# Kernel optimization log

Hardware: AMD Instinct MI355X
Metric: run time of the kernel (lower is better)

## Reference

```python
import jax, jax.numpy as jnp
import numpy as np

D_MODEL = 1024
NUM_HEADS = 16
DEPTH = D_MODEL // NUM_HEADS
B, S = 4, 2048


def setup_inputs() -> dict:
    key = jax.random.key(0)
    ks = jax.random.split(key, 11)
    sc = 1.0 / np.sqrt(D_MODEL)
    return {
        "query": jax.random.normal(ks[0], (B, S, D_MODEL), jnp.float32),
        "key_": jax.random.normal(ks[1], (B, S, D_MODEL), jnp.float32),
        "value": jax.random.normal(ks[2], (B, S, D_MODEL), jnp.float32),
        # torch Linear: y = x @ W.T + b, W shape [out, in]
        "Wq": jax.random.normal(ks[3], (D_MODEL, D_MODEL), jnp.float32) * sc,
        "bq": jax.random.normal(ks[4], (D_MODEL,), jnp.float32) * sc,
        "Wk": jax.random.normal(ks[5], (D_MODEL, D_MODEL), jnp.float32) * sc,
        "bk": jax.random.normal(ks[6], (D_MODEL,), jnp.float32) * sc,
        "Wv": jax.random.normal(ks[7], (D_MODEL, D_MODEL), jnp.float32) * sc,
        "bv": jax.random.normal(ks[8], (D_MODEL,), jnp.float32) * sc,
        "Wo": jax.random.normal(ks[9], (D_MODEL, D_MODEL), jnp.float32) * sc,
        "bo": jax.random.normal(ks[10], (D_MODEL,), jnp.float32) * sc,
    }


def _split_heads(x):
    # [B,S,D] -> [B,H,S,depth]
    b, s, _ = x.shape
    return x.reshape(b, s, NUM_HEADS, DEPTH).transpose(0, 2, 1, 3)


def reference(query, key_, value, Wq, bq, Wk, bk, Wv, bv, Wo, bo):
    Q = _split_heads(query @ Wq.T + bq)
    K = _split_heads(key_ @ Wk.T + bk)
    V = _split_heads(value @ Wv.T + bv)
    scale = 1.0 / jnp.sqrt(jnp.float32(DEPTH))
    scores = jnp.einsum("bhqd,bhkd->bhqk", Q, K) * scale  # [B,H,S,S]
    attention_weights = jax.nn.softmax(scores, axis=-1)
    out = jnp.einsum("bhqk,bhkd->bhqd", attention_weights, V)
    out = out.transpose(0, 2, 1, 3).reshape(query.shape[0], -1, D_MODEL)
    out = out @ Wo.T + bo
    return out, attention_weights
```

## Files before the change

### kernel.cpp

```cpp
#include <hip/hip_runtime.h>

#define NHEAD 16
#define SEQ 2048
#define DMODEL 1024
#define BB 4
#define MROWS (BB*SEQ)
#define NBH (BB*NHEAD)
#define NT (SEQ/32)

typedef float f32x4 __attribute__((ext_vector_type(4)));
typedef _Float16 f16x8 __attribute__((ext_vector_type(8)));
typedef _Float16 f16x4 __attribute__((ext_vector_type(4)));

static __device__ __forceinline__ f32x4 mfma16(f16x8 a, f16x8 b, f32x4 c) {
  return __builtin_amdgcn_mfma_f32_16x16x32_f16(a, b, c, 0, 0, 0);
}

static __device__ __forceinline__ void split2(float x, unsigned short& hi, unsigned short& lo) {
  _Float16 h = (_Float16)x;
  hi = __builtin_bit_cast(unsigned short, h);
  lo = __builtin_bit_cast(unsigned short, (_Float16)(x - (float)h));
}

static __device__ __forceinline__ void gload_lds16(const unsigned short* g, unsigned short* l) {
  __builtin_amdgcn_global_load_lds(
      (const __attribute__((address_space(1))) unsigned int*)g,
      (__attribute__((address_space(3))) unsigned int*)l, 16, 0, 0);
}

__global__ __launch_bounds__(256)
void round_f16(const float* __restrict__ src, unsigned short* __restrict__ dst, int n4)
{
  int i = blockIdx.x*256 + threadIdx.x;
  const int stride = gridDim.x*256;
  for (; i < n4; i += stride) {
    const float4 x = ((const float4*)src)[i];
    ushort4 h;
    h.x = __builtin_bit_cast(unsigned short, (_Float16)x.x);
    h.y = __builtin_bit_cast(unsigned short, (_Float16)x.y);
    h.z = __builtin_bit_cast(unsigned short, (_Float16)x.z);
    h.w = __builtin_bit_cast(unsigned short, (_Float16)x.w);
    ((ushort4*)dst)[i] = h;
  }
}

__global__ __launch_bounds__(256)
void split_f32(const float* __restrict__ src, unsigned short* __restrict__ hi,
               unsigned short* __restrict__ lo, int n4)
{
  int i = blockIdx.x*256 + threadIdx.x;
  const int stride = gridDim.x*256;
  for (; i < n4; i += stride) {
    const float4 x = ((const float4*)src)[i];
    ushort4 h, l;
    split2(x.x, h.x, l.x); split2(x.y, h.y, l.y);
    split2(x.z, h.z, l.z); split2(x.w, h.w, l.w);
    ((ushort4*)hi)[i] = h;
    ((ushort4*)lo)[i] = l;
  }
}

template<int MODE>
__global__ __launch_bounds__(256, 2)
void proj_gemm(const unsigned short* __restrict__ Xf,
               const unsigned short* __restrict__ Wh, const unsigned short* __restrict__ Wl,
               const float* __restrict__ bias, float oscale,
               unsigned short* __restrict__ o16, float* __restrict__ o_f32)
{
  __shared__ unsigned short As[128][32];
  __shared__ unsigned short Bs[128][64];
  const int tid  = threadIdx.x;
  const int wid  = tid >> 6, lane = tid & 63;
  const int g    = lane >> 4, r16 = lane & 15;
  const int id   = blockIdx.y*64 + blockIdx.x;
  const int xcd  = id & 7, slot = id >> 3;
  const int m0   = (xcd*8 + (slot & 7)) * 128;
  const int n0   = (slot >> 3) * 128;
  const int wr   = wid >> 1, wc = wid & 1;

  f32x4 acc[4][4] = {};

  for (int kt = 0; kt < 32; ++kt) {
    const int k0 = kt*32;
    __syncthreads();
#pragma unroll
    for (int r = 0; r < 2; ++r) {
      const int gi = r*256 + tid;
      const int row = gi >> 2, c = gi & 3;
      const int lg = c ^ ((row >> 1) & 3);
      gload_lds16(Xf + (size_t)(m0+row)*DMODEL + k0 + lg*8,
                  &As[0][0] + r*2048 + (tid & 0xC0)*8);
    }
#pragma unroll
    for (int r = 0; r < 4; ++r) {
      const int gi = r*256 + tid;
      const int row = gi >> 3, c = gi & 7;
      const int sg = c ^ (row & 7);
      const unsigned short* src = (sg < 4)
          ? (Wh + (size_t)(n0+row)*DMODEL + k0 + sg*8)
          : (Wl + (size_t)(n0+row)*DMODEL + k0 + (sg-4)*8);
      gload_lds16(src, &Bs[0][0] + r*2048 + (tid & 0xC0)*8);
    }
    asm volatile("s_waitcnt vmcnt(0)" ::: "memory");
    __syncthreads();

    f16x8 a[4], b_h[4], b_l[4];
#pragma unroll
    for (int t = 0; t < 4; ++t) {
      const int ar = wr*64 + t*16 + r16;
      a[t] = *(const f16x8*)((const char*)&As[ar][0] + ((g ^ ((ar >> 1) & 3)) << 4));
      const int br = wc*64 + t*16 + r16;
      const char* pb = (const char*)&Bs[br][0];
      b_h[t] = *(const f16x8*)(pb + (((g    ) ^ (br & 7)) << 4));
      b_l[t] = *(const f16x8*)(pb + (((4 | g) ^ (br & 7)) << 4));
    }
#pragma unroll
    for (int mt = 0; mt < 4; ++mt)
#pragma unroll
      for (int nt = 0; nt < 4; ++nt) {
        acc[mt][nt] = mfma16(a[mt], b_h[nt], acc[mt][nt]);
        acc[mt][nt] = mfma16(a[mt], b_l[nt], acc[mt][nt]);
      }
  }

#pragma unroll
  for (int nt = 0; nt < 4; ++nt) {
    const int n  = n0 + wc*64 + nt*16 + r16;
    const float bn = bias[n];
#pragma unroll
    for (int mt = 0; mt < 4; ++mt) {
      const int mb = m0 + wr*64 + mt*16 + g*4;
      if (MODE == 0) {
#pragma unroll
        for (int j = 0; j < 4; ++j) {
          const int m = mb + j;
          const int bt = m >> 11, s = m & (SEQ-1);
          const int hh = n >> 6,  d = n & 63;
          o16[(((size_t)(bt*NHEAD + hh)*SEQ + s) << 6) + d] =
              __builtin_bit_cast(unsigned short, (_Float16)((acc[mt][nt][j] + bn) * oscale));
        }
      } else if (MODE == 1) {
        const int bt = mb >> 11, sb = mb & (SEQ-1);
        const int hh = n >> 6,  d = n & 63;
        ushort4 v;
        v.x = __builtin_bit_cast(unsigned short, (_Float16)(acc[mt][nt][0] + bn));
        v.y = __builtin_bit_cast(unsigned short, (_Float16)(acc[mt][nt][1] + bn));
        v.z = __builtin_bit_cast(unsigned short, (_Float16)(acc[mt][nt][2] + bn));
        v.w = __builtin_bit_cast(unsigned short, (_Float16)(acc[mt][nt][3] + bn));
        *(ushort4*)(o16 + ((size_t)(bt*NHEAD + hh)*64 + d)*SEQ + sb) = v;
      } else {
#pragma unroll
        for (int j = 0; j < 4; ++j)
          o_f32[(size_t)(mb + j)*DMODEL + n] = acc[mt][nt][j] + bn;
      }
    }
  }
}

static __device__ __forceinline__ void stage_k(unsigned short* dst,
    const unsigned short* __restrict__ Kf, size_t kbase, int k0, int tid)
{
  const int row = tid >> 3, c = tid & 7;
  const int sg = c ^ (row & 7);
  gload_lds16(Kf + kbase + (size_t)(k0+row)*64 + sg*8, dst + (tid & 0xC0)*8);
}

static __device__ __forceinline__ void stage_v(unsigned short* dst,
    const unsigned short* __restrict__ Vtg, int bh, int k0, int tid)
{
  const int row = tid >> 2, c = tid & 3;
  const int lg = c ^ ((row >> 1) & 3);
  gload_lds16(Vtg + ((size_t)bh*64 + row)*SEQ + k0 + lg*8, dst + (tid & 0xC0)*8);
}

__global__ __launch_bounds__(256, 4)
void attn_fused(const unsigned short* __restrict__ Qf, const unsigned short* __restrict__ Kf,
                const unsigned short* __restrict__ Vtg,
                float* __restrict__ wout, unsigned short* __restrict__ of16)
{
  __shared__ unsigned short Ks[4][32][64];
  __shared__ unsigned short Vs[4][64][32];
  __shared__ unsigned short PA[4][16][40];
  const int tid = threadIdx.x, wid = tid >> 6, lane = tid & 63;
  const int g = lane >> 4, r16 = lane & 15;
  const int id = blockIdx.y*32 + blockIdx.x;
  const int xcd = id & 7, slot = id >> 3;
  const int bh = (slot >> 5)*8 + xcd;
  const int bx = slot & 31;
  const int bt = bh >> 4, hh = bh & (NHEAD-1);
  const int s0 = bx*64 + wid*16;
  const size_t kbase = (size_t)bh*SEQ*64;

  const size_t qoff = ((size_t)bh*SEQ + s0 + r16)*64 + (size_t)g*8;
  const f16x8 qh0 = *(const f16x8*)(Qf + qoff);
  const f16x8 qh1 = *(const f16x8*)(Qf + qoff + 32);

  float lp = 0.f;
  stage_k(&Ks[0][0][0], Kf, kbase, 0, tid);
  stage_k(&Ks[1][0][0], Kf, kbase, 32, tid);
  asm volatile("s_waitcnt vmcnt(1)" ::: "memory");
  __builtin_amdgcn_s_barrier();
  for (int kt = 0; kt < NT; ++kt) {
    const int cur = kt & 3;
    const bool pf = kt < NT-2;
    if (pf) stage_k(&Ks[(kt+2)&3][0][0], Kf, kbase, (kt+2)*32, tid);
#pragma unroll
    for (int sub = 0; sub < 2; ++sub) {
      const int krow = sub*16 + r16;
      const char* pk = (const char*)&Ks[cur][krow][0];
      const int sx = krow & 7;
      const f16x8 kh0 = *(const f16x8*)(pk + (((g    ) ^ sx) << 4));
      const f16x8 kh1 = *(const f16x8*)(pk + (((4 | g) ^ sx) << 4));
      f32x4 acc = {};
      __builtin_amdgcn_s_setprio(1);
      acc = mfma16(kh0, qh0, acc);
      acc = mfma16(kh1, qh1, acc);
      __builtin_amdgcn_s_setprio(0);
#pragma unroll
      for (int j = 0; j < 4; ++j) lp += __builtin_exp2f(acc[j]);
    }
    if (pf) { asm volatile("s_waitcnt vmcnt(1)" ::: "memory"); }
    else    { asm volatile("s_waitcnt vmcnt(0)" ::: "memory"); }
    __builtin_amdgcn_s_barrier();
  }
  lp += __shfl_xor(lp, 16);
  lp += __shfl_xor(lp, 32);
  const float li = 1.0f / lp;

  f32x4 acco[4] = {};
  char* paw = (char*)&PA[wid][0][0];

  stage_k(&Ks[0][0][0], Kf, kbase, 0, tid);
  stage_v(&Vs[0][0][0], Vtg, bh, 0, tid);
  stage_k(&Ks[1][0][0], Kf, kbase, 32, tid);
  stage_v(&Vs[1][0][0], Vtg, bh, 32, tid);
  asm volatile("s_waitcnt vmcnt(2)" ::: "memory");
  __builtin_amdgcn_s_barrier();
  for (int kt = 0; kt < NT; ++kt) {
    const int cur = kt & 3;
    const bool pf = kt < NT-2;
    if (pf) {
      stage_k(&Ks[(kt+2)&3][0][0], Kf, kbase, (kt+2)*32, tid);
      stage_v(&Vs[(kt+2)&3][0][0], Vtg, bh, (kt+2)*32, tid);
    }
#pragma unroll
    for (int sub = 0; sub < 2; ++sub) {
      const int krow = sub*16 + r16;
      const char* pk = (const char*)&Ks[cur][krow][0];
      const int sx = krow & 7;
      const f16x8 kh0 = *(const f16x8*)(pk + (((g    ) ^ sx) << 4));
      const f16x8 kh1 = *(const f16x8*)(pk + (((4 | g) ^ sx) << 4));
      f32x4 acc = {};
      __builtin_amdgcn_s_setprio(1);
      acc = mfma16(kh0, qh0, acc);
      acc = mfma16(kh1, qh1, acc);
      __builtin_amdgcn_s_setprio(0);
      f32x4 w4;
      f16x4 p4;
#pragma unroll
      for (int j = 0; j < 4; ++j) {
        w4[j] = __builtin_exp2f(acc[j]) * li;
        p4[j] = (_Float16)w4[j];
      }
      float* wp = wout + ((size_t)bh*SEQ + s0 + r16)*SEQ + kt*32 + sub*16 + 4*g;
      __builtin_nontemporal_store(w4, (f32x4*)wp);
      *(f16x4*)(paw + r16*80 + ((((2*sub + (g >> 1)) ^ (r16 & 3)) << 4) | ((g & 1) << 3))) = p4;
    }
    asm volatile("s_waitcnt lgkmcnt(0)" ::: "memory");
    const f16x8 pa = *(const f16x8*)(paw + r16*80 + ((g ^ (r16 & 3)) << 4));
    __builtin_amdgcn_s_setprio(1);
#pragma unroll
    for (int nt = 0; nt < 4; ++nt) {
      const int vrow = nt*16 + r16;
      const f16x8 vv = *(const f16x8*)((const char*)&Vs[cur][vrow][0] +
                                       ((g ^ ((vrow >> 1) & 3)) << 4));
      acco[nt] = mfma16(pa, vv, acco[nt]);
    }
    __builtin_amdgcn_s_setprio(0);
    if (pf) { asm volatile("s_waitcnt vmcnt(4)" ::: "memory"); }
    else    { asm volatile("s_waitcnt vmcnt(2)" ::: "memory"); }
    __builtin_amdgcn_s_barrier();
  }

#pragma unroll
  for (int nt = 0; nt < 4; ++nt)
#pragma unroll
    for (int j = 0; j < 4; ++j)
      of16[((size_t)bt*SEQ + s0 + 4*g + j)*DMODEL + hh*64 + nt*16 + r16] =
          __builtin_bit_cast(unsigned short, (_Float16)acco[nt][j]);
}

extern "C" void kernel_launch(void* const* d_in, const int* in_sizes, int n_in,
                              void* d_out, int out_size, void* d_ws, size_t ws_size,
                              hipStream_t stream)
{
  const float* query = (const float*)d_in[0];
  const float* key_  = (const float*)d_in[1];
  const float* value = (const float*)d_in[2];
  const float* Wq = (const float*)d_in[3];
  const float* bq = (const float*)d_in[4];
  const float* Wk = (const float*)d_in[5];
  const float* bk = (const float*)d_in[6];
  const float* Wv = (const float*)d_in[7];
  const float* bv = (const float*)d_in[8];
  const float* Wo = (const float*)d_in[9];
  const float* bo = (const float*)d_in[10];

  const size_t NE = (size_t)NBH * SEQ * 64;
  unsigned short* X16 = (unsigned short*)d_ws;
  unsigned short* Qf  = X16 + NE;
  unsigned short* Kf  = Qf + NE;
  unsigned short* Vt  = Kf + NE;
  unsigned short* Of  = Vt + NE;
  unsigned short* WH  = Of + NE;
  unsigned short* WL  = WH + (size_t)DMODEL*DMODEL;

  float* out0  = (float*)d_out;
  float* wattn = out0 + (size_t)MROWS * DMODEL;

  const int nX4 = MROWS*DMODEL/4, nW4 = DMODEL*DMODEL/4;
  const float QSCALE = 0.125f * 1.4426950408889634f;
  dim3 gg(64, 8);

  round_f16<<<1024, 256, 0, stream>>>(query, X16, nX4);
  split_f32<<<512,  256, 0, stream>>>(Wq, WH, WL, nW4);
  proj_gemm<0><<<gg, dim3(256), 0, stream>>>(X16, WH, WL, bq, QSCALE, Qf, nullptr);

  round_f16<<<1024, 256, 0, stream>>>(key_, X16, nX4);
  split_f32<<<512,  256, 0, stream>>>(Wk, WH, WL, nW4);
  proj_gemm<0><<<gg, dim3(256), 0, stream>>>(X16, WH, WL, bk, 1.0f, Kf, nullptr);

  round_f16<<<1024, 256, 0, stream>>>(value, X16, nX4);
  split_f32<<<512,  256, 0, stream>>>(Wv, WH, WL, nW4);
  proj_gemm<1><<<gg, dim3(256), 0, stream>>>(X16, WH, WL, bv, 1.0f, Vt, nullptr);

  attn_fused<<<dim3(32, NBH), dim3(256), 0, stream>>>(Qf, Kf, Vt, wattn, Of);

  split_f32<<<512,  256, 0, stream>>>(Wo, WH, WL, nW4);
  proj_gemm<2><<<gg, dim3(256), 0, stream>>>(Of, WH, WL, bo, 1.0f, nullptr, out0);
}
```

Before: 554.5 us.

## Triple-buffer projection GEMM loads and split attention into row-sum and output kernels

```diff
diff --git a/kernel.cpp b/kernel.cpp
--- a/kernel.cpp
+++ b/kernel.cpp
@@ -60,6 +60,32 @@
   }
 }
 
+static __device__ __forceinline__ void stage_proj(
+    unsigned short* ab, unsigned short* bb,
+    const unsigned short* __restrict__ Xf,
+    const unsigned short* __restrict__ Wh, const unsigned short* __restrict__ Wl,
+    int m0, int n0, int k0, int tid)
+{
+#pragma unroll
+  for (int r = 0; r < 2; ++r) {
+    const int gi = r*256 + tid;
+    const int row = gi >> 2, c = gi & 3;
+    const int lg = c ^ ((row >> 1) & 3);
+    gload_lds16(Xf + (size_t)(m0+row)*DMODEL + k0 + lg*8,
+                ab + r*2048 + (tid & 0xC0)*8);
+  }
+#pragma unroll
+  for (int r = 0; r < 4; ++r) {
+    const int gi = r*256 + tid;
+    const int row = gi >> 3, c = gi & 7;
+    const int sg = c ^ (row & 7);
+    const unsigned short* src = (sg < 4)
+        ? (Wh + (size_t)(n0+row)*DMODEL + k0 + sg*8)
+        : (Wl + (size_t)(n0+row)*DMODEL + k0 + (sg-4)*8);
+    gload_lds16(src, bb + r*2048 + (tid & 0xC0)*8);
+  }
+}
+
 template<int MODE>
 __global__ __launch_bounds__(256, 2)
 void proj_gemm(const unsigned short* __restrict__ Xf,
@@ -67,8 +93,8 @@
                const float* __restrict__ bias, float oscale,
                unsigned short* __restrict__ o16, float* __restrict__ o_f32)
 {
-  __shared__ unsigned short As[128][32];
-  __shared__ unsigned short Bs[128][64];
+  __shared__ unsigned short As[3][128][32];
+  __shared__ unsigned short Bs[3][128][64];
   const int tid  = threadIdx.x;
   const int wid  = tid >> 6, lane = tid & 63;
   const int g    = lane >> 4, r16 = lane & 15;
@@ -80,40 +106,30 @@
 
   f32x4 acc[4][4] = {};
 
+  stage_proj(&As[0][0][0], &Bs[0][0][0], Xf, Wh, Wl, m0, n0, 0,  tid);
+  stage_proj(&As[1][0][0], &Bs[1][0][0], Xf, Wh, Wl, m0, n0, 32, tid);
+  asm volatile("s_waitcnt vmcnt(6)" ::: "memory");
+  __builtin_amdgcn_s_barrier();
+
+  int bsel = 0;
   for (int kt = 0; kt < 32; ++kt) {
-    const int k0 = kt*32;
-    __syncthreads();
-#pragma unroll
-    for (int r = 0; r < 2; ++r) {
-      const int gi = r*256 + tid;
-      const int row = gi >> 2, c = gi & 3;
-      const int lg = c ^ ((row >> 1) & 3);
-      gload_lds16(Xf + (size_t)(m0+row)*DMODEL + k0 + lg*8,
-                  &As[0][0] + r*2048 + (tid & 0xC0)*8);
-    }
-#pragma unroll
-    for (int r = 0; r < 4; ++r) {
-      const int gi = r*256 + tid;
-      const int row = gi >> 3, c = gi & 7;
-      const int sg = c ^ (row & 7);
-      const unsigned short* src = (sg < 4)
-          ? (Wh + (size_t)(n0+row)*DMODEL + k0 + sg*8)
-          : (Wl + (size_t)(n0+row)*DMODEL + k0 + (sg-4)*8);
-      gload_lds16(src, &Bs[0][0] + r*2048 + (tid & 0xC0)*8);
-    }
-    asm volatile("s_waitcnt vmcnt(0)" ::: "memory");
-    __syncthreads();
-
+    int bnx = bsel + 2; if (bnx >= 3) bnx -= 3;
+    if (kt < 30)
+      stage_proj(&As[bnx][0][0], &Bs[bnx][0][0], Xf, Wh, Wl, m0, n0, (kt+2)*32, tid);
+
+    const unsigned short (*Asb)[32] = As[bsel];
+    const unsigned short (*Bsb)[64] = Bs[bsel];
     f16x8 a[4], b_h[4], b_l[4];
 #pragma unroll
     for (int t = 0; t < 4; ++t) {
       const int ar = wr*64 + t*16 + r16;
-      a[t] = *(const f16x8*)((const char*)&As[ar][0] + ((g ^ ((ar >> 1) & 3)) << 4));
+      a[t] = *(const f16x8*)((const char*)&Asb[ar][0] + ((g ^ ((ar >> 1) & 3)) << 4));
       const int br = wc*64 + t*16 + r16;
-      const char* pb = (const char*)&Bs[br][0];
+      const char* pb = (const char*)&Bsb[br][0];
       b_h[t] = *(const f16x8*)(pb + (((g    ) ^ (br & 7)) << 4));
       b_l[t] = *(const f16x8*)(pb + (((4 | g) ^ (br & 7)) << 4));
     }
+    __builtin_amdgcn_s_setprio(1);
 #pragma unroll
     for (int mt = 0; mt < 4; ++mt)
 #pragma unroll
@@ -121,6 +137,16 @@
         acc[mt][nt] = mfma16(a[mt], b_h[nt], acc[mt][nt]);
         acc[mt][nt] = mfma16(a[mt], b_l[nt], acc[mt][nt]);
       }
+    __builtin_amdgcn_s_setprio(0);
+
+    if (kt < 30) {
+      asm volatile("s_waitcnt vmcnt(6)" ::: "memory");
+      __builtin_amdgcn_s_barrier();
+    } else if (kt == 30) {
+      asm volatile("s_waitcnt vmcnt(0)" ::: "memory");
+      __builtin_amdgcn_s_barrier();
+    }
+    bsel = bsel + 1; if (bsel >= 3) bsel = 0;
   }
 
 #pragma unroll
@@ -173,10 +199,76 @@
   gload_lds16(Vtg + ((size_t)bh*64 + row)*SEQ + k0 + lg*8, dst + (tid & 0xC0)*8);
 }
 
+__global__ __launch_bounds__(256, 6)
+void attn_l(const unsigned short* __restrict__ Qf, const unsigned short* __restrict__ Kf,
+            float* __restrict__ lrow)
+{
+  __shared__ unsigned short Ks[6][32][64];
+  const int tid = threadIdx.x, wid = tid >> 6, lane = tid & 63;
+  const int g = lane >> 4, r16 = lane & 15;
+  const int id = blockIdx.y*32 + blockIdx.x;
+  const int xcd = id & 7, slot = id >> 3;
+  const int bh = (slot >> 5)*8 + xcd;
+  const int bx = slot & 31;
+  const int s0 = bx*64 + wid*16;
+  const size_t kbase = (size_t)bh*SEQ*64;
+
+  const size_t qoff = ((size_t)bh*SEQ + s0 + r16)*64 + (size_t)g*8;
+  const f16x8 qh0 = *(const f16x8*)(Qf + qoff);
+  const f16x8 qh1 = *(const f16x8*)(Qf + qoff + 32);
+
+  float lp = 0.f;
+  stage_k(&Ks[0][0][0], Kf, kbase, 0,  tid);
+  stage_k(&Ks[1][0][0], Kf, kbase, 32, tid);
+  stage_k(&Ks[2][0][0], Kf, kbase, 64, tid);
+  stage_k(&Ks[3][0][0], Kf, kbase, 96, tid);
+  asm volatile("s_waitcnt vmcnt(2)" ::: "memory");
+  __builtin_amdgcn_s_barrier();
+
+  int b0 = 0;
+  for (int c = 0; c < 32; ++c) {
+    if (c < 30) {
+      int bn = b0 + 4; if (bn >= 6) bn -= 6;
+      stage_k(&Ks[bn  ][0][0], Kf, kbase, (c+2)*64,      tid);
+      stage_k(&Ks[bn+1][0][0], Kf, kbase, (c+2)*64 + 32, tid);
+    }
+#pragma unroll
+    for (int t = 0; t < 2; ++t) {
+      const unsigned short (*Kt)[64] = Ks[b0 + t];
+#pragma unroll
+      for (int sub = 0; sub < 2; ++sub) {
+        const int krow = sub*16 + r16;
+        const char* pk = (const char*)&Kt[krow][0];
+        const int sx = krow & 7;
+        const f16x8 kh0 = *(const f16x8*)(pk + (((g    ) ^ sx) << 4));
+        const f16x8 kh1 = *(const f16x8*)(pk + (((4 | g) ^ sx) << 4));
+        f32x4 acc = {};
+        __builtin_amdgcn_s_setprio(1);
+        acc = mfma16(kh0, qh0, acc);
+        acc = mfma16(kh1, qh1, acc);
+        __builtin_amdgcn_s_setprio(0);
+#pragma unroll
+        for (int j = 0; j < 4; ++j) lp += __builtin_exp2f(acc[j]);
+      }
+    }
+    if (c < 30) {
+      asm volatile("s_waitcnt vmcnt(2)" ::: "memory");
+      __builtin_amdgcn_s_barrier();
+    } else if (c == 30) {
+      asm volatile("s_waitcnt vmcnt(0)" ::: "memory");
+      __builtin_amdgcn_s_barrier();
+    }
+    b0 += 2; if (b0 >= 6) b0 = 0;
+  }
+  lp += __shfl_xor(lp, 16);
+  lp += __shfl_xor(lp, 32);
+  if (lane < 16) lrow[(size_t)bh*SEQ + s0 + r16] = 1.0f / lp;
+}
+
 __global__ __launch_bounds__(256, 4)
-void attn_fused(const unsigned short* __restrict__ Qf, const unsigned short* __restrict__ Kf,
-                const unsigned short* __restrict__ Vtg,
-                float* __restrict__ wout, unsigned short* __restrict__ of16)
+void attn_wv(const unsigned short* __restrict__ Qf, const unsigned short* __restrict__ Kf,
+             const unsigned short* __restrict__ Vtg, const float* __restrict__ lrow,
+             float* __restrict__ wout, unsigned short* __restrict__ of16)
 {
   __shared__ unsigned short Ks[4][32][64];
   __shared__ unsigned short Vs[4][64][32];
@@ -194,38 +286,7 @@
   const size_t qoff = ((size_t)bh*SEQ + s0 + r16)*64 + (size_t)g*8;
   const f16x8 qh0 = *(const f16x8*)(Qf + qoff);
   const f16x8 qh1 = *(const f16x8*)(Qf + qoff + 32);
-
-  float lp = 0.f;
-  stage_k(&Ks[0][0][0], Kf, kbase, 0, tid);
-  stage_k(&Ks[1][0][0], Kf, kbase, 32, tid);
-  asm volatile("s_waitcnt vmcnt(1)" ::: "memory");
-  __builtin_amdgcn_s_barrier();
-  for (int kt = 0; kt < NT; ++kt) {
-    const int cur = kt & 3;
-    const bool pf = kt < NT-2;
-    if (pf) stage_k(&Ks[(kt+2)&3][0][0], Kf, kbase, (kt+2)*32, tid);
-#pragma unroll
-    for (int sub = 0; sub < 2; ++sub) {
-      const int krow = sub*16 + r16;
-      const char* pk = (const char*)&Ks[cur][krow][0];
-      const int sx = krow & 7;
-      const f16x8 kh0 = *(const f16x8*)(pk + (((g    ) ^ sx) << 4));
-      const f16x8 kh1 = *(const f16x8*)(pk + (((4 | g) ^ sx) << 4));
-      f32x4 acc = {};
-      __builtin_amdgcn_s_setprio(1);
-      acc = mfma16(kh0, qh0, acc);
-      acc = mfma16(kh1, qh1, acc);
-      __builtin_amdgcn_s_setprio(0);
-#pragma unroll
-      for (int j = 0; j < 4; ++j) lp += __builtin_exp2f(acc[j]);
-    }
-    if (pf) { asm volatile("s_waitcnt vmcnt(1)" ::: "memory"); }
-    else    { asm volatile("s_waitcnt vmcnt(0)" ::: "memory"); }
-    __builtin_amdgcn_s_barrier();
-  }
-  lp += __shfl_xor(lp, 16);
-  lp += __shfl_xor(lp, 32);
-  const float li = 1.0f / lp;
+  const float li = lrow[(size_t)bh*SEQ + s0 + r16];
 
   f32x4 acco[4] = {};
   char* paw = (char*)&PA[wid][0][0];
@@ -236,10 +297,10 @@
   stage_v(&Vs[1][0][0], Vtg, bh, 32, tid);
   asm volatile("s_waitcnt vmcnt(2)" ::: "memory");
   __builtin_amdgcn_s_barrier();
+
   for (int kt = 0; kt < NT; ++kt) {
     const int cur = kt & 3;
-    const bool pf = kt < NT-2;
-    if (pf) {
+    if (kt < NT-2) {
       stage_k(&Ks[(kt+2)&3][0][0], Kf, kbase, (kt+2)*32, tid);
       stage_v(&Vs[(kt+2)&3][0][0], Vtg, bh, (kt+2)*32, tid);
     }
@@ -277,9 +338,13 @@
       acco[nt] = mfma16(pa, vv, acco[nt]);
     }
     __builtin_amdgcn_s_setprio(0);
-    if (pf) { asm volatile("s_waitcnt vmcnt(4)" ::: "memory"); }
-    else    { asm volatile("s_waitcnt vmcnt(2)" ::: "memory"); }
-    __builtin_amdgcn_s_barrier();
+    if (kt == 0) {
+      asm volatile("s_waitcnt vmcnt(4)" ::: "memory"); __builtin_amdgcn_s_barrier();
+    } else if (kt < NT-2) {
+      asm volatile("s_waitcnt vmcnt(6)" ::: "memory"); __builtin_amdgcn_s_barrier();
+    } else if (kt == NT-2) {
+      asm volatile("s_waitcnt vmcnt(4)" ::: "memory"); __builtin_amdgcn_s_barrier();
+    }
   }
 
 #pragma unroll
@@ -314,6 +379,7 @@
   unsigned short* Of  = Vt + NE;
   unsigned short* WH  = Of + NE;
   unsigned short* WL  = WH + (size_t)DMODEL*DMODEL;
+  float* lrow = (float*)(WL + (size_t)DMODEL*DMODEL);
 
   float* out0  = (float*)d_out;
   float* wattn = out0 + (size_t)MROWS * DMODEL;
@@ -334,7 +400,8 @@
   split_f32<<<512,  256, 0, stream>>>(Wv, WH, WL, nW4);
   proj_gemm<1><<<gg, dim3(256), 0, stream>>>(X16, WH, WL, bv, 1.0f, Vt, nullptr);
 
-  attn_fused<<<dim3(32, NBH), dim3(256), 0, stream>>>(Qf, Kf, Vt, wattn, Of);
+  attn_l <<<dim3(32, NBH), dim3(256), 0, stream>>>(Qf, Kf, lrow);
+  attn_wv<<<dim3(32, NBH), dim3(256), 0, stream>>>(Qf, Kf, Vt, lrow, wattn, Of);
 
   split_f32<<<512,  256, 0, stream>>>(Wo, WH, WL, nW4);
   proj_gemm<2><<<gg, dim3(256), 0, stream>>>(Of, WH, WL, bo, 1.0f, nullptr, out0);
```

Measured after the change: 635.9 us. +14.7%, slower.

## Double-buffer projection GEMM LDS tiles and retune attention wait counts

Applied to the files above, without the earlier changes.

```diff
diff --git a/kernel.cpp b/kernel.cpp
--- a/kernel.cpp
+++ b/kernel.cpp
@@ -60,15 +60,41 @@
   }
 }
 
+static __device__ __forceinline__ void stage_proj(
+    unsigned short* ab, unsigned short* bb,
+    const unsigned short* __restrict__ Xf,
+    const unsigned short* __restrict__ Wh, const unsigned short* __restrict__ Wl,
+    int m0, int n0, int k0, int tid)
+{
+#pragma unroll
+  for (int r = 0; r < 2; ++r) {
+    const int gi = r*256 + tid;
+    const int row = gi >> 2, c = gi & 3;
+    const int lg = c ^ ((row >> 1) & 3);
+    gload_lds16(Xf + (size_t)(m0+row)*DMODEL + k0 + lg*8,
+                ab + r*2048 + (tid & 0xC0)*8);
+  }
+#pragma unroll
+  for (int r = 0; r < 4; ++r) {
+    const int gi = r*256 + tid;
+    const int row = gi >> 3, c = gi & 7;
+    const int sg = c ^ (row & 7);
+    const unsigned short* src = (sg < 4)
+        ? (Wh + (size_t)(n0+row)*DMODEL + k0 + sg*8)
+        : (Wl + (size_t)(n0+row)*DMODEL + k0 + (sg-4)*8);
+    gload_lds16(src, bb + r*2048 + (tid & 0xC0)*8);
+  }
+}
+
 template<int MODE>
-__global__ __launch_bounds__(256, 2)
+__global__ __launch_bounds__(256, 3)
 void proj_gemm(const unsigned short* __restrict__ Xf,
                const unsigned short* __restrict__ Wh, const unsigned short* __restrict__ Wl,
                const float* __restrict__ bias, float oscale,
                unsigned short* __restrict__ o16, float* __restrict__ o_f32)
 {
-  __shared__ unsigned short As[128][32];
-  __shared__ unsigned short Bs[128][64];
+  __shared__ unsigned short As[2][128][32];
+  __shared__ unsigned short Bs[2][128][64];
   const int tid  = threadIdx.x;
   const int wid  = tid >> 6, lane = tid & 63;
   const int g    = lane >> 4, r16 = lane & 15;
@@ -80,40 +106,28 @@
 
   f32x4 acc[4][4] = {};
 
+  stage_proj(&As[0][0][0], &Bs[0][0][0], Xf, Wh, Wl, m0, n0, 0, tid);
+  asm volatile("s_waitcnt vmcnt(0)" ::: "memory");
+  __builtin_amdgcn_s_barrier();
+
   for (int kt = 0; kt < 32; ++kt) {
-    const int k0 = kt*32;
-    __syncthreads();
-#pragma unroll
-    for (int r = 0; r < 2; ++r) {
-      const int gi = r*256 + tid;
-      const int row = gi >> 2, c = gi & 3;
-      const int lg = c ^ ((row >> 1) & 3);
-      gload_lds16(Xf + (size_t)(m0+row)*DMODEL + k0 + lg*8,
-                  &As[0][0] + r*2048 + (tid & 0xC0)*8);
-    }
-#pragma unroll
-    for (int r = 0; r < 4; ++r) {
-      const int gi = r*256 + tid;
-      const int row = gi >> 3, c = gi & 7;
-      const int sg = c ^ (row & 7);
-      const unsigned short* src = (sg < 4)
-          ? (Wh + (size_t)(n0+row)*DMODEL + k0 + sg*8)
-          : (Wl + (size_t)(n0+row)*DMODEL + k0 + (sg-4)*8);
-      gload_lds16(src, &Bs[0][0] + r*2048 + (tid & 0xC0)*8);
-    }
-    asm volatile("s_waitcnt vmcnt(0)" ::: "memory");
-    __syncthreads();
-
+    const int cur = kt & 1;
+    if (kt < 31)
+      stage_proj(&As[cur^1][0][0], &Bs[cur^1][0][0], Xf, Wh, Wl, m0, n0, (kt+1)*32, tid);
+
+    const unsigned short (*Asb)[32] = As[cur];
+    const unsigned short (*Bsb)[64] = Bs[cur];
     f16x8 a[4], b_h[4], b_l[4];
 #pragma unroll
     for (int t = 0; t < 4; ++t) {
       const int ar = wr*64 + t*16 + r16;
-      a[t] = *(const f16x8*)((const char*)&As[ar][0] + ((g ^ ((ar >> 1) & 3)) << 4));
+      a[t] = *(const f16x8*)((const char*)&Asb[ar][0] + ((g ^ ((ar >> 1) & 3)) << 4));
       const int br = wc*64 + t*16 + r16;
-      const char* pb = (const char*)&Bs[br][0];
+      const char* pb = (const char*)&Bsb[br][0];
       b_h[t] = *(const f16x8*)(pb + (((g    ) ^ (br & 7)) << 4));
       b_l[t] = *(const f16x8*)(pb + (((4 | g) ^ (br & 7)) << 4));
     }
+    __builtin_amdgcn_s_setprio(1);
 #pragma unroll
     for (int mt = 0; mt < 4; ++mt)
 #pragma unroll
@@ -121,6 +135,12 @@
         acc[mt][nt] = mfma16(a[mt], b_h[nt], acc[mt][nt]);
         acc[mt][nt] = mfma16(a[mt], b_l[nt], acc[mt][nt]);
       }
+    __builtin_amdgcn_s_setprio(0);
+
+    if (kt < 31) {
+      asm volatile("s_waitcnt vmcnt(0)" ::: "memory");
+      __builtin_amdgcn_s_barrier();
+    }
   }
 
 #pragma unroll
@@ -238,8 +258,7 @@
   __builtin_amdgcn_s_barrier();
   for (int kt = 0; kt < NT; ++kt) {
     const int cur = kt & 3;
-    const bool pf = kt < NT-2;
-    if (pf) {
+    if (kt < NT-2) {
       stage_k(&Ks[(kt+2)&3][0][0], Kf, kbase, (kt+2)*32, tid);
       stage_v(&Vs[(kt+2)&3][0][0], Vtg, bh, (kt+2)*32, tid);
     }
@@ -277,9 +296,13 @@
       acco[nt] = mfma16(pa, vv, acco[nt]);
     }
     __builtin_amdgcn_s_setprio(0);
-    if (pf) { asm volatile("s_waitcnt vmcnt(4)" ::: "memory"); }
-    else    { asm volatile("s_waitcnt vmcnt(2)" ::: "memory"); }
-    __builtin_amdgcn_s_barrier();
+    if (kt == 0) {
+      asm volatile("s_waitcnt vmcnt(4)" ::: "memory"); __builtin_amdgcn_s_barrier();
+    } else if (kt < NT-2) {
+      asm volatile("s_waitcnt vmcnt(6)" ::: "memory"); __builtin_amdgcn_s_barrier();
+    } else if (kt == NT-2) {
+      asm volatile("s_waitcnt vmcnt(4)" ::: "memory"); __builtin_amdgcn_s_barrier();
+    }
   }
 
 #pragma unroll
```

New measurement: 558.3 us. About the same (+0.7%).
